# Performance work log

Measured on AMD Instinct MI355X. Metric: run time of the kernel, lower is better.

The kernel has to match this reference:

```python
import jax, jax.numpy as jnp
import numpy as np

N_MEM = 500_000
D_LATENT = 512
D_QUERY = 768


def setup_inputs() -> dict:
    key = jax.random.key(0)
    ks = jax.random.split(key, 8)
    s = 1.0 / np.sqrt(D_QUERY)
    s2 = 1.0 / np.sqrt(2 * D_LATENT)
    s3 = 1.0 / np.sqrt(D_LATENT)
    return {
        "query": jax.random.normal(ks[0], (D_QUERY,), dtype=jnp.float32),
        "memory": jax.random.normal(ks[1], (N_MEM, D_LATENT), dtype=jnp.float32),
        "Wp": jax.random.uniform(ks[2], (D_LATENT, D_QUERY), jnp.float32, -s, s),
        "bp": jax.random.uniform(ks[3], (D_LATENT,), jnp.float32, -s, s),
        "W1": jax.random.uniform(ks[4], (D_LATENT, 2 * D_LATENT), jnp.float32, -s2, s2),
        "b1": jax.random.uniform(ks[5], (D_LATENT,), jnp.float32, -s2, s2),
        "W2": jax.random.uniform(ks[6], (1, D_LATENT), jnp.float32, -s3, s3),
        "b2": jax.random.uniform(ks[7], (1,), jnp.float32, -s3, s3),
        "k": 16,
    }


def reference(query, memory, Wp, bp, W1, b1, W2, b2, k):
    # query projection: [d_query] -> [d_latent]
    q = Wp @ query + bp  # [D_LATENT]
    # memory bank retrieve: cosine similarity, top 2k candidates
    qn = q / (jnp.linalg.norm(q) + 1e-8)
    mn = memory / (jnp.linalg.norm(memory, axis=-1, keepdims=True) + 1e-8)
    sims = mn @ qn  # [N_MEM]
    _, cand_idx = jax.lax.top_k(sims, 2 * k)  # [2k]
    cand = memory[cand_idx]  # [2k, D_LATENT]
    # batched rerank MLP: concat(query_latent, candidate) -> Linear -> ReLU -> Linear
    combined = jnp.concatenate(
        [jnp.broadcast_to(q, (2 * k, D_LATENT)), cand], axis=-1
    )  # [2k, 2*D_LATENT]
    h = jax.nn.relu(combined @ W1.T + b1)  # [2k, D_LATENT]
    scores = (h @ W2.T + b2)[:, 0]  # [2k]
    # sort by rerank score (desc), keep top k
    top_scores, sel = jax.lax.top_k(scores, k)
    return top_scores, cand_idx[sel]
```

## Files before the change

### kernel.cpp

```cpp
#include <hip/hip_runtime.h>
#include <hip/hip_bf16.h>
#include <math.h>

static constexpr size_t SIMS_OFF   = 0;
static constexpr size_t Q_OFF      = 500736;
static constexpr size_t QN_OFF     = 501248;
static constexpr size_t HIST_OFF   = 501760;
static constexpr size_t COUNT_OFF  = 505856;
static constexpr size_t THRESH_OFF = 505872;
static constexpr size_t CANDV_OFF  = 505888;
static constexpr size_t CANDI_OFF  = 514080;
static constexpr size_t SELI_OFF   = 522272;
static constexpr size_t SELV_OFF   = 522304;
static constexpr size_t COMB_OFF   = 522336;
static constexpr size_t H_OFF      = 555104;

static constexpr int D_LAT   = 512;
static constexpr int D_QRY   = 768;
static constexpr int NBUCKET = 4096;
static constexpr int CAND_CAP= 8192;
static constexpr int K2      = 32;
static constexpr int K1      = 16;

__global__ __launch_bounds__(512) void k_proj(
    const float* __restrict__ Wp, const float* __restrict__ query,
    const float* __restrict__ bp, float* __restrict__ q, float* __restrict__ qn) {
  const int tid  = threadIdx.x;
  const int lane = tid & 63;
  const int wave = tid >> 6;
  __shared__ float s_q[D_LAT];
  __shared__ float s_red[512];

  const float4* q4 = (const float4*)query;
  float4 qq0 = q4[lane*3+0], qq1 = q4[lane*3+1], qq2 = q4[lane*3+2];

  for (int i = wave; i < D_LAT; i += 8) {
    const float4* w4 = (const float4*)(Wp + (size_t)i * D_QRY);
    float4 w0 = w4[lane*3+0], w1 = w4[lane*3+1], w2 = w4[lane*3+2];
    float acc = w0.x*qq0.x + w0.y*qq0.y + w0.z*qq0.z + w0.w*qq0.w
              + w1.x*qq1.x + w1.y*qq1.y + w1.z*qq1.z + w1.w*qq1.w
              + w2.x*qq2.x + w2.y*qq2.y + w2.z*qq2.z + w2.w*qq2.w;
#pragma unroll
    for (int off = 32; off; off >>= 1) acc += __shfl_xor(acc, off, 64);
    if (lane == 0) {
      float v = acc + bp[i];
      s_q[i] = v;
      q[i]   = v;
    }
  }
  __syncthreads();

  float v = s_q[tid];
  s_red[tid] = v * v;
  __syncthreads();
  for (int s = 256; s > 0; s >>= 1) {
    if (tid < s) s_red[tid] += s_red[tid + s];
    __syncthreads();
  }
  float nrm = sqrtf(s_red[0]) + 1e-8f;
  qn[tid] = v / nrm;
}

__global__ __launch_bounds__(256) void k_sims(
    const float* __restrict__ mem, const float* __restrict__ qn,
    float* __restrict__ sims, unsigned* __restrict__ ghist, int nrows) {
  __shared__ unsigned hist[NBUCKET];
  for (int i = threadIdx.x; i < NBUCKET; i += 256) hist[i] = 0;
  __syncthreads();

  const int lane   = threadIdx.x & 63;
  const int wave   = (blockIdx.x * 256 + threadIdx.x) >> 6;
  const int nwaves = (gridDim.x * 256) >> 6;

  const float4* qn4 = (const float4*)qn;
  float4 qa = qn4[lane*2], qb = qn4[lane*2+1];

  for (int row = wave; row < nrows; row += nwaves) {
    const float4* m4 = (const float4*)(mem + (size_t)row * D_LAT);
    float4 a = m4[lane*2], b = m4[lane*2+1];
    float dot = a.x*qa.x + a.y*qa.y + a.z*qa.z + a.w*qa.w
              + b.x*qb.x + b.y*qb.y + b.z*qb.z + b.w*qb.w;
    float ss  = a.x*a.x + a.y*a.y + a.z*a.z + a.w*a.w
              + b.x*b.x + b.y*b.y + b.z*b.z + b.w*b.w;
#pragma unroll
    for (int off = 32; off; off >>= 1) {
      dot += __shfl_xor(dot, off, 64);
      ss  += __shfl_xor(ss,  off, 64);
    }
    if (lane == 0) {
      float s = dot / (sqrtf(ss) + 1e-8f);
      sims[row] = s;
      int bkt = (int)((s + 1.0f) * 2048.0f);
      bkt = bkt < 0 ? 0 : (bkt > NBUCKET-1 ? NBUCKET-1 : bkt);
      atomicAdd(&hist[bkt], 1u);
    }
  }
  __syncthreads();
  for (int i = threadIdx.x; i < NBUCKET; i += 256)
    if (hist[i]) atomicAdd(&ghist[i], hist[i]);
}

__global__ void k_thresh(const unsigned* __restrict__ ghist, float* __restrict__ thresh) {
  if (threadIdx.x == 0 && blockIdx.x == 0) {
    unsigned c = 0; int b = NBUCKET - 1;
    for (; b >= 0; --b) { c += ghist[b]; if (c >= (unsigned)K2) break; }
    if (b < 0) b = 0;
    thresh[0] = (float)b * (1.0f/2048.0f) - 1.0f - 1e-6f;
  }
}

__global__ __launch_bounds__(256) void k_collect(
    const float* __restrict__ sims, const float* __restrict__ thresh,
    float* __restrict__ cv, int* __restrict__ ci, unsigned* __restrict__ count, int n) {
  float t = thresh[0];
  int stride = gridDim.x * 256;
  for (int i = blockIdx.x * 256 + threadIdx.x; i < n; i += stride) {
    float v = sims[i];
    if (v >= t) {
      unsigned p = atomicAdd(count, 1u);
      if (p < (unsigned)CAND_CAP) { cv[p] = v; ci[p] = i; }
    }
  }
}

__global__ __launch_bounds__(256) void k_select(
    const float* __restrict__ cv, const int* __restrict__ ci,
    const unsigned* __restrict__ count, const float* __restrict__ q,
    const float* __restrict__ mem, int* __restrict__ seli,
    float* __restrict__ selv, float* __restrict__ comb) {
  __shared__ int   s_idx[K2];
  __shared__ float s_val[K2];
  if (threadIdx.x == 0) {
    int n = (int)(*count);
    if (n > CAND_CAP) n = CAND_CAP;
    float pv = 1e30f; int pi = -1;
    for (int s = 0; s < K2; ++s) {
      float bv = -1e30f; int bi = 0x7fffffff;
      for (int j = 0; j < n; ++j) {
        float v = cv[j]; int id = ci[j];
        if (v > pv || (v == pv && id <= pi)) continue;
        if (v > bv || (v == bv && id < bi)) { bv = v; bi = id; }
      }
      s_val[s] = bv; s_idx[s] = bi;
      pv = bv; pi = bi;
    }
  }
  __syncthreads();
  if (threadIdx.x < K2) { seli[threadIdx.x] = s_idx[threadIdx.x]; selv[threadIdx.x] = s_val[threadIdx.x]; }
  for (int t = threadIdx.x; t < K2 * 2 * D_LAT; t += 256) {
    int c = t >> 10, j = t & 1023;
    comb[t] = (j < D_LAT) ? q[j] : mem[(size_t)s_idx[c] * D_LAT + (j - D_LAT)];
  }
}

__global__ __launch_bounds__(256) void k_mlp1(
    const float* __restrict__ comb, const float* __restrict__ W1,
    const float* __restrict__ b1, float* __restrict__ h) {
  int t = blockIdx.x * 256 + threadIdx.x;
  int c = t & 31, i = t >> 5;
  const float4* w4 = (const float4*)(W1 + (size_t)i * (2*D_LAT));
  const float4* c4 = (const float4*)(comb + (size_t)c * (2*D_LAT));
  float acc = 0.f;
#pragma unroll 8
  for (int j = 0; j < (2*D_LAT)/4; ++j) {
    float4 w = w4[j], x = c4[j];
    acc += w.x*x.x + w.y*x.y + w.z*x.z + w.w*x.w;
  }
  acc += b1[i];
  h[(size_t)c * D_LAT + i] = fmaxf(acc, 0.f);
}

__global__ __launch_bounds__(64) void k_final(
    const float* __restrict__ h, const float* __restrict__ W2,
    const float* __restrict__ b2, const int* __restrict__ seli,
    float* __restrict__ out) {
  __shared__ float sc[K2];
  if (threadIdx.x < K2) {
    const float* hr = h + (size_t)threadIdx.x * D_LAT;
    float acc = 0.f;
    for (int i = 0; i < D_LAT; ++i) acc += hr[i] * W2[i];
    sc[threadIdx.x] = acc + b2[0];
  }
  __syncthreads();
  if (threadIdx.x == 0) {
    float pv = 1e30f; int pc = -1;
    for (int s = 0; s < K1; ++s) {
      float bv = -1e30f; int bc = 0;
      for (int c = 0; c < K2; ++c) {
        float v = sc[c];
        if (v > pv || (v == pv && c <= pc)) continue;
        if (v > bv) { bv = v; bc = c; }
      }
      out[s]      = bv;
      out[K1 + s] = (float)seli[bc];
      pv = bv; pc = bc;
    }
  }
}

extern "C" void kernel_launch(void* const* d_in, const int* in_sizes, int n_in,
                              void* d_out, int out_size, void* d_ws, size_t ws_size,
                              hipStream_t stream) {
  (void)n_in; (void)out_size; (void)ws_size;
  const float* query  = (const float*)d_in[0];
  const float* memory = (const float*)d_in[1];
  const float* Wp     = (const float*)d_in[2];
  const float* bp     = (const float*)d_in[3];
  const float* W1     = (const float*)d_in[4];
  const float* b1     = (const float*)d_in[5];
  const float* W2     = (const float*)d_in[6];
  const float* b2     = (const float*)d_in[7];
  const int nrows = in_sizes[1] / D_LAT;

  float*    ws    = (float*)d_ws;
  float*    sims  = ws + SIMS_OFF;
  float*    q     = ws + Q_OFF;
  float*    qn    = ws + QN_OFF;
  unsigned* hist  = (unsigned*)(ws + HIST_OFF);
  unsigned* count = (unsigned*)(ws + COUNT_OFF);
  float*    thr   = ws + THRESH_OFF;
  float*    candv = ws + CANDV_OFF;
  int*      candi = (int*)(ws + CANDI_OFF);
  int*      seli  = (int*)(ws + SELI_OFF);
  float*    selv  = ws + SELV_OFF;
  float*    comb  = ws + COMB_OFF;
  float*    h     = ws + H_OFF;
  float*    out   = (float*)d_out;

  hipMemsetAsync(hist, 0, (NBUCKET + 16) * sizeof(unsigned), stream);
  k_proj   <<<1,    512, 0, stream>>>(Wp, query, bp, q, qn);
  k_sims   <<<4096, 256, 0, stream>>>(memory, qn, sims, hist, nrows);
  k_thresh <<<1,     64, 0, stream>>>(hist, thr);
  k_collect<<<256,  256, 0, stream>>>(sims, thr, candv, candi, count, nrows);
  k_select <<<1,    256, 0, stream>>>(candv, candi, count, q, memory, seli, selv, comb);
  k_mlp1   <<<64,   256, 0, stream>>>(comb, W1, b1, h);
  k_final  <<<1,     64, 0, stream>>>(h, W2, b2, seli, out);
}
```

Baseline: 1.664 ms.

## Parallelize projection, threshold scan, final scoring; drop per-block LDS histogram

Splits the query projection across many blocks with a separate norm kernel. It replaces the per-block shared histogram in the similarity kernel with direct global atomics. The threshold search becomes a wave-parallel suffix scan, candidates are staged in LDS for selection, and the final scoring is spread over 256 threads. This targets serial single-thread sections and the per-block histogram init/flush overhead, at the cost of more global atomic contention and an extra launch.

Measured after the change: 1.916 ms. 15.1% more time.

```diff
diff --git a/kernel.cpp b/kernel.cpp
--- a/kernel.cpp
+++ b/kernel.cpp
@@ -19,55 +19,44 @@
 static constexpr int D_QRY   = 768;
 static constexpr int NBUCKET = 4096;
 static constexpr int CAND_CAP= 8192;
+static constexpr int LDS_CAP = 4096;
 static constexpr int K2      = 32;
 static constexpr int K1      = 16;
 
-__global__ __launch_bounds__(512) void k_proj(
+__global__ __launch_bounds__(256) void k_proj(
     const float* __restrict__ Wp, const float* __restrict__ query,
-    const float* __restrict__ bp, float* __restrict__ q, float* __restrict__ qn) {
-  const int tid  = threadIdx.x;
-  const int lane = tid & 63;
-  const int wave = tid >> 6;
-  __shared__ float s_q[D_LAT];
-  __shared__ float s_red[512];
-
+    const float* __restrict__ bp, float* __restrict__ q) {
+  const int lane = threadIdx.x & 63;
+  const int row  = blockIdx.x * 4 + (threadIdx.x >> 6);
   const float4* q4 = (const float4*)query;
   float4 qq0 = q4[lane*3+0], qq1 = q4[lane*3+1], qq2 = q4[lane*3+2];
-
-  for (int i = wave; i < D_LAT; i += 8) {
-    const float4* w4 = (const float4*)(Wp + (size_t)i * D_QRY);
-    float4 w0 = w4[lane*3+0], w1 = w4[lane*3+1], w2 = w4[lane*3+2];
-    float acc = w0.x*qq0.x + w0.y*qq0.y + w0.z*qq0.z + w0.w*qq0.w
-              + w1.x*qq1.x + w1.y*qq1.y + w1.z*qq1.z + w1.w*qq1.w
-              + w2.x*qq2.x + w2.y*qq2.y + w2.z*qq2.z + w2.w*qq2.w;
-#pragma unroll
-    for (int off = 32; off; off >>= 1) acc += __shfl_xor(acc, off, 64);
-    if (lane == 0) {
-      float v = acc + bp[i];
-      s_q[i] = v;
-      q[i]   = v;
-    }
-  }
-  __syncthreads();
-
-  float v = s_q[tid];
+  const float4* w4 = (const float4*)(Wp + (size_t)row * D_QRY);
+  float4 w0 = w4[lane*3+0], w1 = w4[lane*3+1], w2 = w4[lane*3+2];
+  float acc = w0.x*qq0.x + w0.y*qq0.y + w0.z*qq0.z + w0.w*qq0.w
+            + w1.x*qq1.x + w1.y*qq1.y + w1.z*qq1.z + w1.w*qq1.w
+            + w2.x*qq2.x + w2.y*qq2.y + w2.z*qq2.z + w2.w*qq2.w;
+#pragma unroll
+  for (int off = 32; off; off >>= 1) acc += __shfl_xor(acc, off, 64);
+  if (lane == 0) q[row] = acc + bp[row];
+}
+
+__global__ __launch_bounds__(512) void k_norm(
+    const float* __restrict__ q, float* __restrict__ qn) {
+  __shared__ float s_red[512];
+  int tid = threadIdx.x;
+  float v = q[tid];
   s_red[tid] = v * v;
   __syncthreads();
   for (int s = 256; s > 0; s >>= 1) {
     if (tid < s) s_red[tid] += s_red[tid + s];
     __syncthreads();
   }
-  float nrm = sqrtf(s_red[0]) + 1e-8f;
-  qn[tid] = v / nrm;
+  qn[tid] = v / (sqrtf(s_red[0]) + 1e-8f);
 }
 
 __global__ __launch_bounds__(256) void k_sims(
     const float* __restrict__ mem, const float* __restrict__ qn,
     float* __restrict__ sims, unsigned* __restrict__ ghist, int nrows) {
-  __shared__ unsigned hist[NBUCKET];
-  for (int i = threadIdx.x; i < NBUCKET; i += 256) hist[i] = 0;
-  __syncthreads();
-
   const int lane   = threadIdx.x & 63;
   const int wave   = (blockIdx.x * 256 + threadIdx.x) >> 6;
   const int nwaves = (gridDim.x * 256) >> 6;
@@ -92,20 +81,38 @@
       sims[row] = s;
       int bkt = (int)((s + 1.0f) * 2048.0f);
       bkt = bkt < 0 ? 0 : (bkt > NBUCKET-1 ? NBUCKET-1 : bkt);
-      atomicAdd(&hist[bkt], 1u);
-    }
-  }
-  __syncthreads();
-  for (int i = threadIdx.x; i < NBUCKET; i += 256)
-    if (hist[i]) atomicAdd(&ghist[i], hist[i]);
-}
-
-__global__ void k_thresh(const unsigned* __restrict__ ghist, float* __restrict__ thresh) {
-  if (threadIdx.x == 0 && blockIdx.x == 0) {
-    unsigned c = 0; int b = NBUCKET - 1;
-    for (; b >= 0; --b) { c += ghist[b]; if (c >= (unsigned)K2) break; }
-    if (b < 0) b = 0;
-    thresh[0] = (float)b * (1.0f/2048.0f) - 1.0f - 1e-6f;
+      atomicAdd(&ghist[bkt], 1u);
+    }
+  }
+}
+
+__global__ __launch_bounds__(64) void k_thresh(
+    const unsigned* __restrict__ ghist, float* __restrict__ thresh) {
+  __shared__ unsigned s_h[NBUCKET];
+  const int lane = threadIdx.x;
+  unsigned csum = 0;
+#pragma unroll 8
+  for (int j = 0; j < 64; ++j) {
+    unsigned v = ghist[lane * 64 + j];
+    s_h[lane * 64 + j] = v;
+    csum += v;
+  }
+  unsigned suf = csum;
+#pragma unroll
+  for (int off = 1; off < 64; off <<= 1) {
+    unsigned t = __shfl_down(suf, off, 64);
+    if (lane + off < 64) suf += t;
+  }
+  unsigned above = suf - csum;
+  if (lane == 0 && suf < (unsigned)K2) thresh[0] = -2.0f;
+  if (above < (unsigned)K2 && suf >= (unsigned)K2) {
+    unsigned cum = above;
+    int b = lane * 64;
+    for (int j = 63; j >= 0; --j) {
+      cum += s_h[lane * 64 + j];
+      if (cum >= (unsigned)K2) { b = lane * 64 + j; break; }
+    }
+    thresh[0] = (float)b * (1.0f / 2048.0f) - 1.0f - 1e-6f;
   }
 }
 
@@ -128,16 +135,24 @@
     const unsigned* __restrict__ count, const float* __restrict__ q,
     const float* __restrict__ mem, int* __restrict__ seli,
     float* __restrict__ selv, float* __restrict__ comb) {
+  __shared__ float s_v[LDS_CAP];
+  __shared__ int   s_i[LDS_CAP];
   __shared__ int   s_idx[K2];
   __shared__ float s_val[K2];
+  int n = (int)(*count);
+  if (n > CAND_CAP) n = CAND_CAP;
+  const bool lds_ok = (n <= LDS_CAP);
+  if (lds_ok) {
+    for (int i = threadIdx.x; i < n; i += 256) { s_v[i] = cv[i]; s_i[i] = ci[i]; }
+  }
+  __syncthreads();
   if (threadIdx.x == 0) {
-    int n = (int)(*count);
-    if (n > CAND_CAP) n = CAND_CAP;
     float pv = 1e30f; int pi = -1;
     for (int s = 0; s < K2; ++s) {
       float bv = -1e30f; int bi = 0x7fffffff;
       for (int j = 0; j < n; ++j) {
-        float v = cv[j]; int id = ci[j];
+        float v  = lds_ok ? s_v[j] : cv[j];
+        int   id = lds_ok ? s_i[j] : ci[j];
         if (v > pv || (v == pv && id <= pi)) continue;
         if (v > bv || (v == bv && id < bi)) { bv = v; bi = id; }
       }
@@ -170,26 +185,37 @@
   h[(size_t)c * D_LAT + i] = fmaxf(acc, 0.f);
 }
 
-__global__ __launch_bounds__(64) void k_final(
+__global__ __launch_bounds__(256) void k_final(
     const float* __restrict__ h, const float* __restrict__ W2,
     const float* __restrict__ b2, const int* __restrict__ seli,
     float* __restrict__ out) {
+  __shared__ float part[256];
   __shared__ float sc[K2];
-  if (threadIdx.x < K2) {
-    const float* hr = h + (size_t)threadIdx.x * D_LAT;
-    float acc = 0.f;
-    for (int i = 0; i < D_LAT; ++i) acc += hr[i] * W2[i];
-    sc[threadIdx.x] = acc + b2[0];
-  }
-  __syncthreads();
-  if (threadIdx.x == 0) {
+  const int t = threadIdx.x;
+  const int c = t >> 3, p = t & 7;
+  const float4* hr = (const float4*)(h + (size_t)c * D_LAT + p * 64);
+  const float4* w  = (const float4*)(W2 + p * 64);
+  float acc = 0.f;
+#pragma unroll
+  for (int j = 0; j < 16; ++j) {
+    float4 a = hr[j], b = w[j];
+    acc += a.x*b.x + a.y*b.y + a.z*b.z + a.w*b.w;
+  }
+  part[t] = acc;
+  __syncthreads();
+  if (p == 0) {
+    float s = part[t]+part[t+1]+part[t+2]+part[t+3]+part[t+4]+part[t+5]+part[t+6]+part[t+7];
+    sc[c] = s + b2[0];
+  }
+  __syncthreads();
+  if (t == 0) {
     float pv = 1e30f; int pc = -1;
     for (int s = 0; s < K1; ++s) {
       float bv = -1e30f; int bc = 0;
-      for (int c = 0; c < K2; ++c) {
-        float v = sc[c];
-        if (v > pv || (v == pv && c <= pc)) continue;
-        if (v > bv) { bv = v; bc = c; }
+      for (int c2 = 0; c2 < K2; ++c2) {
+        float v = sc[c2];
+        if (v > pv || (v == pv && c2 <= pc)) continue;
+        if (v > bv) { bv = v; bc = c2; }
       }
       out[s]      = bv;
       out[K1 + s] = (float)seli[bc];
@@ -228,11 +254,12 @@
   float*    out   = (float*)d_out;
 
   hipMemsetAsync(hist, 0, (NBUCKET + 16) * sizeof(unsigned), stream);
-  k_proj   <<<1,    512, 0, stream>>>(Wp, query, bp, q, qn);
+  k_proj   <<<128,  256, 0, stream>>>(Wp, query, bp, q);
+  k_norm   <<<1,    512, 0, stream>>>(q, qn);
   k_sims   <<<4096, 256, 0, stream>>>(memory, qn, sims, hist, nrows);
   k_thresh <<<1,     64, 0, stream>>>(hist, thr);
   k_collect<<<256,  256, 0, stream>>>(sims, thr, candv, candi, count, nrows);
   k_select <<<1,    256, 0, stream>>>(candv, candi, count, q, memory, seli, selv, comb);
   k_mlp1   <<<64,   256, 0, stream>>>(comb, W1, b1, h);
-  k_final  <<<1,     64, 0, stream>>>(h, W2, b2, seli, out);
-}
+  k_final  <<<1,    256, 0, stream>>>(h, W2, b2, seli, out);
+}
```
